# Kernel tuning notes

Measured on AMD Instinct MI355X. Metric: run time of the kernel, lower is better.

## Reference

```python
import jax, jax.numpy as jnp
import numpy as np

B, L, D, H = 8, 512, 512, 8
E, G = 4, 2            # primary experts, ghost experts
THRESH = 0.01          # ghost_activation_threshold
EPS = 1e-5             # LayerNorm eps (torch default)


def _ln(x, s, b):
    m = x.mean(-1, keepdims=True)
    v = ((x - m) ** 2).mean(-1, keepdims=True)
    return (x - m) * jax.lax.rsqrt(v + EPS) * s + b


def _expert(x, ln1_s, ln1_b, wqkv, bqkv, wo, bo, ln2_s, ln2_b, w1, b1, w2, b2):
    # Pre-norm transformer block: MHA + residual, FFN + residual (dropout=0)
    Bn, Ln, Dn = x.shape
    dh = Dn // H
    xn = _ln(x, ln1_s, ln1_b)
    qkv = xn @ wqkv + bqkv                      # [B,L,3D]
    q, k, v = jnp.split(qkv, 3, axis=-1)
    heads = lambda t: t.reshape(Bn, Ln, H, dh).transpose(0, 2, 1, 3)
    q, k, v = heads(q), heads(k), heads(v)      # [B,H,L,dh]
    scores = jnp.einsum('bhqd,bhkd->bhqk', q, k) / np.sqrt(dh).astype(np.float32)
    attn = jax.nn.softmax(scores, axis=-1)
    o = jnp.einsum('bhqk,bhkd->bhqd', attn, v).transpose(0, 2, 1, 3).reshape(Bn, Ln, Dn)
    x = x + o @ wo + bo
    h = _ln(x, ln2_s, ln2_b)
    x = x + jax.nn.gelu(h @ w1 + b1) @ w2 + b2
    return x


def _make_params(key, n, d):
    ks = jax.random.split(key, 4)
    s = 0.02
    return dict(
        ln1_s=jnp.ones((n, d)), ln1_b=jnp.zeros((n, d)),
        wqkv=jax.random.normal(ks[0], (n, d, 3 * d)) * s, bqkv=jnp.zeros((n, 3 * d)),
        wo=jax.random.normal(ks[1], (n, d, d)) * s, bo=jnp.zeros((n, d)),
        ln2_s=jnp.ones((n, d)), ln2_b=jnp.zeros((n, d)),
        w1=jax.random.normal(ks[2], (n, d, 4 * d)) * s, b1=jnp.zeros((n, 4 * d)),
        w2=jax.random.normal(ks[3], (n, 4 * d, d)) * s, b2=jnp.zeros((n, d)))


def setup_inputs() -> dict:
    key = jax.random.key(0)
    k1, k2, k3 = jax.random.split(key, 3)
    inp = {'x': jax.random.normal(k1, (B, L, D), jnp.float32), 'step': 100}
    for pre, n, k in (('p_', E, k2), ('g_', G, k3)):
        for name, arr in _make_params(k, n, D).items():
            inp[pre + name] = arr
    return inp


def reference(x, step,
              p_ln1_s, p_ln1_b, p_wqkv, p_bqkv, p_wo, p_bo, p_ln2_s, p_ln2_b, p_w1, p_b1, p_w2, p_b2,
              g_ln1_s, g_ln1_b, g_wqkv, g_bqkv, g_wo, g_bo, g_ln2_s, g_ln2_b, g_w1, g_b1, g_w2, g_b2):
    pp = (p_ln1_s, p_ln1_b, p_wqkv, p_bqkv, p_wo, p_bo, p_ln2_s, p_ln2_b, p_w1, p_b1, p_w2, p_b2)
    gp = (g_ln1_s, g_ln1_b, g_wqkv, g_bqkv, g_wo, g_bo, g_ln2_s, g_ln2_b, g_w1, g_b1, g_w2, g_b2)
    run = jax.vmap(lambda ps: _expert(x, *ps))
    prim = run(pp)                               # [E,B,L,D]
    # --- saturation metrics (statistics only; detached like .item() in torch) ---
    mean_eo = prim.mean(axis=(1, 2))             # [E,D]
    nrm = mean_eo / jnp.linalg.norm(mean_eo, axis=1, keepdims=True)
    gram = nrm @ nrm.T                           # [E,E]
    ortho = 1.0 - jnp.mean((gram - jnp.eye(E, dtype=gram.dtype)) ** 2)
    recon = prim.mean(axis=0)                    # [B,L,D]
    uvar = jnp.var(x - recon, ddof=1)            # torch.var unbiased default
    sat = jax.lax.stop_gradient(ortho * uvar)
    # --- ghost activation (initial state: all dormant -> ghost 0 gets 0.01) ---
    base = jnp.zeros((G,), x.dtype).at[0].set(0.01)
    rates = jnp.where(sat > THRESH, base, jnp.zeros((G,), x.dtype))
    ghost = jax.vmap(lambda ps: _expert(x, *ps))(gp) * rates[:, None, None, None]  # [G,B,L,D]
    # combine: mean over all (primary + ghost) expert outputs
    out = jnp.concatenate([prim, ghost], axis=0).mean(axis=0)  # [B,L,D]
    return out
```

## Files before the change

### kernel.cpp

```cpp
#include <hip/hip_runtime.h>

typedef __bf16 bf16;
typedef __bf16 bf16x8 __attribute__((ext_vector_type(8)));
typedef float  f32x4  __attribute__((ext_vector_type(4)));

#define AS1 __attribute__((address_space(1)))
#define AS3 __attribute__((address_space(3)))

__device__ __forceinline__ void async16(const void* g, void* l) {
  __builtin_amdgcn_global_load_lds((const AS1 unsigned int*)g, (AS3 unsigned int*)l, 16, 0, 0);
}

__device__ __forceinline__ float gelu_fast(float u) {
  float z = 0.7978845608028654f * (u + 0.044715f * u * u * u);
  z = fminf(fmaxf(z, -15.f), 15.f);
  float t = __expf(2.f * z);
  return u * t / (t + 1.f);
}

template <int FOLD>
__global__ __launch_bounds__(256) void transpose_cvt(
    const float* pbase, const float* gbase, bf16* dst, int K, int M,
    const float* lnsP, const float* lnbP, const float* lnsG, const float* lnbG,
    const float* b0P, const float* b0G, float* bias_eff) {
  __shared__ float tile[32][33];
  const int z = blockIdx.z;
  const float* src = (z < 4) ? pbase + (size_t)z * K * M : gbase;
  bf16* d = dst + (size_t)z * M * K;
  const int mBlk = blockIdx.x * 32, kBlk = blockIdx.y * 32;
  const int tx = threadIdx.x, ty = threadIdx.y;
  for (int i = 0; i < 4; i++)
    tile[ty + i * 8][tx] = src[(size_t)(kBlk + ty + i * 8) * M + mBlk + tx];
  __syncthreads();
  if constexpr (FOLD) {
    const float* s  = (z < 4) ? lnsP + (size_t)z * 512 : lnsG;
    const float* bb = (z < 4) ? lnbP + (size_t)z * 512 : lnbG;
    const float sk = s[kBlk + tx];
    for (int i = 0; i < 4; i++)
      d[(size_t)(mBlk + ty + i * 8) * K + kBlk + tx] = (bf16)(tile[tx][ty + i * 8] * sk);
    if (ty == 0) {
      float acc = 0.f;
      for (int kk = 0; kk < 32; kk++) acc += bb[kBlk + kk] * tile[kk][tx];
      if (kBlk == 0) {
        const float* b0 = (z < 4) ? b0P + (size_t)z * M : b0G;
        acc += b0[mBlk + tx];
      }
      atomicAdd(&bias_eff[(size_t)z * M + mBlk + tx], acc);
    }
  } else {
    for (int i = 0; i < 4; i++)
      d[(size_t)(mBlk + ty + i * 8) * K + kBlk + tx] = (bf16)tile[tx][ty + i * 8];
  }
}

__global__ __launch_bounds__(256) void ln_plain(const float* x, bf16* out) {
  const int t = blockIdx.x, tid = threadIdx.x;
  const float* xr = x + (size_t)t * 512;
  float v0 = xr[tid], v1 = xr[tid + 256];
  float s1 = v0 + v1, s2 = v0 * v0 + v1 * v1;
  for (int off = 32; off > 0; off >>= 1) { s1 += __shfl_down(s1, off); s2 += __shfl_down(s2, off); }
  __shared__ float red[8];
  __shared__ float mv[2];
  if ((tid & 63) == 0) { red[tid >> 6] = s1; red[4 + (tid >> 6)] = s2; }
  __syncthreads();
  if (tid == 0) {
    float a = red[0] + red[1] + red[2] + red[3];
    float b = red[4] + red[5] + red[6] + red[7];
    float mean = a * (1.f / 512.f);
    float var = b * (1.f / 512.f) - mean * mean;
    mv[0] = mean; mv[1] = 1.f / sqrtf(var + 1e-5f);
  }
  __syncthreads();
  const float mean = mv[0], rs = mv[1];
  bf16* o = out + (size_t)t * 512;
  o[tid]       = (bf16)((v0 - mean) * rs);
  o[tid + 256] = (bf16)((v1 - mean) * rs);
}

__global__ __launch_bounds__(256) void ln2_kernel(const bf16* in, const float* sP, const float* bP,
                                                  const float* sG, const float* bG, bf16* out) {
  const int t = blockIdx.x, z = blockIdx.y, tid = threadIdx.x;
  const bf16* xr = in + (size_t)z * 4096 * 512 + (size_t)t * 512;
  float v0 = (float)xr[tid], v1 = (float)xr[tid + 256];
  float s1 = v0 + v1, s2 = v0 * v0 + v1 * v1;
  for (int off = 32; off > 0; off >>= 1) { s1 += __shfl_down(s1, off); s2 += __shfl_down(s2, off); }
  __shared__ float red[8];
  __shared__ float mv[2];
  if ((tid & 63) == 0) { red[tid >> 6] = s1; red[4 + (tid >> 6)] = s2; }
  __syncthreads();
  if (tid == 0) {
    float a = red[0] + red[1] + red[2] + red[3];
    float b = red[4] + red[5] + red[6] + red[7];
    float mean = a * (1.f / 512.f);
    float var = b * (1.f / 512.f) - mean * mean;
    mv[0] = mean; mv[1] = 1.f / sqrtf(var + 1e-5f);
  }
  __syncthreads();
  const float mean = mv[0], rs = mv[1];
  const float* sc = (z < 4) ? sP + (size_t)z * 512 : sG;
  const float* bi = (z < 4) ? bP + (size_t)z * 512 : bG;
  bf16* o = out + (size_t)z * 4096 * 512 + (size_t)t * 512;
  o[tid]       = (bf16)((v0 - mean) * rs * sc[tid] + bi[tid]);
  o[tid + 256] = (bf16)((v1 - mean) * rs * sc[tid + 256] + bi[tid + 256]);
}

template <int MODE>
__global__ __launch_bounds__(256, 2) void gemm_bt(
    const bf16* Abase, long long aStrideZ, const bf16* Wt,
    const float* biasP, const float* biasG, int K, int M,
    bf16* out, const void* resid, long long residStrideZ) {
  const int bx = blockIdx.x, by = blockIdx.y, z = blockIdx.z;
  const bf16* A = Abase + (size_t)z * aStrideZ;
  const bf16* B = Wt + (size_t)z * M * K;
  const float* bias = (z < 4) ? biasP + (size_t)z * M : biasG;
  __shared__ bf16 smem[128 * 136];
  bf16* As = smem;
  bf16* Bs = smem + 128 * 64;
  const int tid = threadIdx.x, wave = tid >> 6, l = tid & 63;
  const int m16 = l & 15, q4 = l >> 4;
  const int wm = wave & 1, wn = wave >> 1;
  f32x4 zero4 = {0.f, 0.f, 0.f, 0.f};
  f32x4 acc[4][4];
  for (int i = 0; i < 4; i++) for (int j = 0; j < 4; j++) acc[i][j] = zero4;
  const int rowA0 = by * 128, rowB0 = bx * 128;

  for (int kt = 0; kt < K; kt += 64) {
    __syncthreads();
    for (int i = 0; i < 4; i++) {
      int s = i * 256 + tid, r = s >> 3, kb = s & 7;
      int col = kt + ((kb ^ (r & 7)) << 3);
      async16(A + (size_t)(rowA0 + r) * K + col, &As[(i * 256 + wave * 64) * 8]);
      async16(B + (size_t)(rowB0 + r) * K + col, &Bs[(i * 256 + wave * 64) * 8]);
    }
    __syncthreads();
    for (int ks = 0; ks < 2; ks++) {
      bf16x8 af[4], bfr[4];
      for (int mi = 0; mi < 4; mi++) {
        int r = wm * 64 + mi * 16 + m16, kb = ks * 4 + q4;
        af[mi] = *(const bf16x8*)&As[r * 64 + ((kb ^ (r & 7)) << 3)];
      }
      for (int ni = 0; ni < 4; ni++) {
        int r = wn * 64 + ni * 16 + m16, kb = ks * 4 + q4;
        bfr[ni] = *(const bf16x8*)&Bs[r * 64 + ((kb ^ (r & 7)) << 3)];
      }
      for (int mi = 0; mi < 4; mi++)
        for (int ni = 0; ni < 4; ni++)
          acc[mi][ni] = __builtin_amdgcn_mfma_f32_16x16x32_bf16(af[mi], bfr[ni], acc[mi][ni], 0, 0, 0);
    }
  }

  __syncthreads();
  for (int ni = 0; ni < 4; ni++) {
    int coll = wn * 64 + ni * 16 + m16;
    float bb = bias[rowB0 + coll];
    for (int mi = 0; mi < 4; mi++) {
      for (int cr = 0; cr < 4; cr++) {
        float v = acc[mi][ni][cr] + bb;
        if constexpr (MODE == 2) v = gelu_fast(v);
        smem[(wm * 64 + mi * 16 + q4 * 4 + cr) * 136 + coll] = (bf16)v;
      }
    }
  }
  __syncthreads();
  bf16* ob = out + (size_t)z * 4096 * M;
  for (int p = 0; p < 8; p++) {
    int r = p * 16 + (tid >> 4), c0 = (tid & 15) * 8;
    bf16x8 vv = *(const bf16x8*)&smem[r * 136 + c0];
    if constexpr (MODE == 1) {
      const float* rx = (const float*)resid + (size_t)(rowA0 + r) * 512 + rowB0 + c0;
      for (int j = 0; j < 8; j++) vv[j] = (bf16)((float)vv[j] + rx[j]);
    } else if constexpr (MODE == 3) {
      const bf16* rx = (const bf16*)resid + (size_t)z * residStrideZ + (size_t)(rowA0 + r) * 512 + rowB0 + c0;
      bf16x8 rv = *(const bf16x8*)rx;
      for (int j = 0; j < 8; j++) vv[j] = (bf16)((float)vv[j] + (float)rv[j]);
    }
    *(bf16x8*)&ob[(size_t)(rowA0 + r) * M + rowB0 + c0] = vv;
  }
}

__global__ __launch_bounds__(256, 2) void attn_kernel(const bf16* qkv, bf16* o) {
  const int qt = blockIdx.x, bh = blockIdx.y, z = blockIdx.z;
  const int b = bh >> 3, h = bh & 7;
  const bf16* base = qkv + (size_t)z * 4096 * 1536 + (size_t)b * 512 * 1536;
  __shared__ bf16 Qs[128 * 64];
  __shared__ bf16 Ks[64 * 64];
  __shared__ bf16 Vt[64 * 72];
  __shared__ bf16 Ps[4][32 * 72];
  const int tid = threadIdx.x, wave = tid >> 6, l = tid & 63;
  const int m16 = l & 15, q4 = l >> 4;
  f32x4 zero4 = {0.f, 0.f, 0.f, 0.f};

  for (int i = 0; i < 4; i++) {
    int s = i * 256 + tid, r = s >> 3, kb = s & 7;
    async16(base + (size_t)(qt * 128 + r) * 1536 + h * 64 + ((kb ^ (r & 7)) << 3),
            &Qs[(i * 256 + wave * 64) * 8]);
  }
  f32x4 Oacc[2][4];
  float m_run[2][4], l_run[2][4];
  for (int rt = 0; rt < 2; rt++)
    for (int cr = 0; cr < 4; cr++) { m_run[rt][cr] = -3.0e38f; l_run[rt][cr] = 0.f; }
  for (int rt = 0; rt < 2; rt++) for (int dt = 0; dt < 4; dt++) Oacc[rt][dt] = zero4;
  __syncthreads();
  bf16x8 qf[2][2];
  for (int rt = 0; rt < 2; rt++)
    for (int ks = 0; ks < 2; ks++) {
      int r = wave * 32 + rt * 16 + m16, kb = ks * 4 + q4;
      qf[rt][ks] = *(const bf16x8*)&Qs[r * 64 + ((kb ^ (r & 7)) << 3)];
    }

  for (int kt = 0; kt < 8; kt++) {
    __syncthreads();
    for (int i = 0; i < 2; i++) {
      int s = i * 256 + tid, r = s >> 3, kb = s & 7;
      async16(base + (size_t)(kt * 64 + r) * 1536 + 512 + h * 64 + ((kb ^ (r & 7)) << 3),
              &Ks[(i * 256 + wave * 64) * 8]);
    }
    for (int p = 0; p < 2; p++) {
      int k = p * 32 + (tid >> 3), d0 = (tid & 7) * 8;
      bf16x8 v8 = *(const bf16x8*)&base[(size_t)(kt * 64 + k) * 1536 + 1024 + h * 64 + d0];
      for (int j = 0; j < 8; j++) Vt[(d0 + j) * 72 + k] = v8[j];
    }
    __syncthreads();
    f32x4 S[2][4];
    for (int rt = 0; rt < 2; rt++)
      for (int ct = 0; ct < 4; ct++) {
        f32x4 a = zero4;
        for (int ks = 0; ks < 2; ks++) {
          int n = ct * 16 + m16, kb = ks * 4 + q4;
          bf16x8 kf = *(const bf16x8*)&Ks[n * 64 + ((kb ^ (n & 7)) << 3)];
          a = __builtin_amdgcn_mfma_f32_16x16x32_bf16(qf[rt][ks], kf, a, 0, 0, 0);
        }
        S[rt][ct] = a * 0.125f;
      }
    float alpha[2][4];
    for (int rt = 0; rt < 2; rt++)
      for (int cr = 0; cr < 4; cr++) {
        float mx = fmaxf(fmaxf(S[rt][0][cr], S[rt][1][cr]), fmaxf(S[rt][2][cr], S[rt][3][cr]));
        mx = fmaxf(mx, __shfl_xor(mx, 1)); mx = fmaxf(mx, __shfl_xor(mx, 2));
        mx = fmaxf(mx, __shfl_xor(mx, 4)); mx = fmaxf(mx, __shfl_xor(mx, 8));
        float mnew = fmaxf(m_run[rt][cr], mx);
        float al = __expf(m_run[rt][cr] - mnew);
        m_run[rt][cr] = mnew;
        float rs = 0.f;
        for (int ct = 0; ct < 4; ct++) {
          float p = __expf(S[rt][ct][cr] - mnew);
          S[rt][ct][cr] = p; rs += p;
        }
        rs += __shfl_xor(rs, 1); rs += __shfl_xor(rs, 2);
        rs += __shfl_xor(rs, 4); rs += __shfl_xor(rs, 8);
        l_run[rt][cr] = l_run[rt][cr] * al + rs;
        alpha[rt][cr] = al;
      }
    for (int rt = 0; rt < 2; rt++)
      for (int dt = 0; dt < 4; dt++)
        for (int cr = 0; cr < 4; cr++) Oacc[rt][dt][cr] *= alpha[rt][cr];
    bf16* pw = &Ps[wave][0];
    for (int rt = 0; rt < 2; rt++)
      for (int ct = 0; ct < 4; ct++)
        for (int cr = 0; cr < 4; cr++)
          pw[(rt * 16 + q4 * 4 + cr) * 72 + ct * 16 + m16] = (bf16)S[rt][ct][cr];
    for (int rt = 0; rt < 2; rt++)
      for (int dt = 0; dt < 4; dt++) {
        f32x4 a = Oacc[rt][dt];
        for (int ks = 0; ks < 2; ks++) {
          bf16x8 pf = *(const bf16x8*)&pw[(rt * 16 + m16) * 72 + ks * 32 + q4 * 8];
          bf16x8 vf = *(const bf16x8*)&Vt[(dt * 16 + m16) * 72 + ks * 32 + q4 * 8];
          a = __builtin_amdgcn_mfma_f32_16x16x32_bf16(pf, vf, a, 0, 0, 0);
        }
        Oacc[rt][dt] = a;
      }
  }
  bf16* ob = o + (size_t)z * 4096 * 512 + (size_t)(b * 512 + qt * 128 + wave * 32) * 512 + h * 64;
  for (int rt = 0; rt < 2; rt++)
    for (int dt = 0; dt < 4; dt++)
      for (int cr = 0; cr < 4; cr++) {
        int r = rt * 16 + q4 * 4 + cr;
        ob[(size_t)r * 512 + dt * 16 + m16] = (bf16)(Oacc[rt][dt][cr] / l_run[rt][cr]);
      }
}

__global__ __launch_bounds__(256) void stats_k(const bf16* eout, const float* x,
                                               float* prim_sum, float* mean_acc, float* accum) {
  const int r0 = blockIdx.x * 32;
  const int tid = threadIdx.x;
  const int c0 = tid * 2;
  float cs[4][2] = {{0.f,0.f},{0.f,0.f},{0.f,0.f},{0.f,0.f}};
  float sd = 0.f, sd2 = 0.f;
  for (int rr = 0; rr < 32; rr++) {
    int row = r0 + rr;
    float s0 = 0.f, s1 = 0.f;
    for (int e = 0; e < 4; e++) {
      const bf16* p = &eout[((size_t)e * 4096 + row) * 512 + c0];
      float f0 = (float)p[0], f1 = (float)p[1];
      cs[e][0] += f0; cs[e][1] += f1;
      s0 += f0; s1 += f1;
    }
    prim_sum[(size_t)row * 512 + c0]     = s0;
    prim_sum[(size_t)row * 512 + c0 + 1] = s1;
    float d0 = x[(size_t)row * 512 + c0]     - s0 * 0.25f;
    float d1 = x[(size_t)row * 512 + c0 + 1] - s1 * 0.25f;
    sd += d0 + d1; sd2 += d0 * d0 + d1 * d1;
  }
  for (int e = 0; e < 4; e++) {
    atomicAdd(&mean_acc[e * 512 + c0],     cs[e][0]);
    atomicAdd(&mean_acc[e * 512 + c0 + 1], cs[e][1]);
  }
  for (int off = 32; off > 0; off >>= 1) { sd += __shfl_down(sd, off); sd2 += __shfl_down(sd2, off); }
  __shared__ float r1[4], r2[4];
  if ((tid & 63) == 0) { r1[tid >> 6] = sd; r2[tid >> 6] = sd2; }
  __syncthreads();
  if (tid == 0) {
    atomicAdd(&accum[0], r1[0] + r1[1] + r1[2] + r1[3]);
    atomicAdd(&accum[1], r2[0] + r2[1] + r2[2] + r2[3]);
  }
}

__global__ void finalize_k(const float* mean_acc, const float* accum, float* rate) {
  const int l = threadIdx.x;
  float me[4][8];
  for (int e = 0; e < 4; e++)
    for (int j = 0; j < 8; j++) me[e][j] = mean_acc[e * 512 + l * 8 + j] * (1.f / 4096.f);
  float dot[4][4];
  for (int e = 0; e < 4; e++)
    for (int f = e; f < 4; f++) {
      float d = 0.f;
      for (int j = 0; j < 8; j++) d += me[e][j] * me[f][j];
      for (int off = 32; off > 0; off >>= 1) d += __shfl_xor(d, off);
      dot[e][f] = d; dot[f][e] = d;
    }
  float nrm[4];
  for (int e = 0; e < 4; e++) nrm[e] = sqrtf(dot[e][e]);
  float acc = 0.f;
  for (int e = 0; e < 4; e++)
    for (int f = 0; f < 4; f++) {
      float g = dot[e][f] / (nrm[e] * nrm[f]) - (e == f ? 1.f : 0.f);
      acc += g * g;
    }
  float ortho = 1.f - acc * (1.f / 16.f);
  float n = 2097152.f;
  float uvar = (accum[1] - accum[0] * accum[0] / n) / (n - 1.f);
  float sat = ortho * uvar;
  if (l == 0) rate[0] = (sat > 0.01f) ? 0.01f : 0.f;
}

__global__ __launch_bounds__(256) void combine_k(const float* prim, const bf16* ghost,
                                                 const float* rate, float* out) {
  float r = rate[0];
  int i = blockIdx.x * 256 + threadIdx.x;
  f32x4 p = ((const f32x4*)prim)[i];
  const bf16* g = ghost + (size_t)i * 4;
  f32x4 o;
  for (int j = 0; j < 4; j++) o[j] = (p[j] + r * (float)g[j]) * (1.f / 6.f);
  ((f32x4*)out)[i] = o;
}

extern "C" void kernel_launch(void* const* d_in, const int* in_sizes, int n_in,
                              void* d_out, int out_size, void* d_ws, size_t ws_size,
                              hipStream_t stream) {
  const float* x       = (const float*)d_in[0];
  const float* p_ln1_s = (const float*)d_in[2];
  const float* p_ln1_b = (const float*)d_in[3];
  const float* p_wqkv  = (const float*)d_in[4];
  const float* p_bqkv  = (const float*)d_in[5];
  const float* p_wo    = (const float*)d_in[6];
  const float* p_bo    = (const float*)d_in[7];
  const float* p_ln2_s = (const float*)d_in[8];
  const float* p_ln2_b = (const float*)d_in[9];
  const float* p_w1    = (const float*)d_in[10];
  const float* p_b1    = (const float*)d_in[11];
  const float* p_w2    = (const float*)d_in[12];
  const float* p_b2    = (const float*)d_in[13];
  const float* g_ln1_s = (const float*)d_in[14];
  const float* g_ln1_b = (const float*)d_in[15];
  const float* g_wqkv  = (const float*)d_in[16];
  const float* g_bqkv  = (const float*)d_in[17];
  const float* g_wo    = (const float*)d_in[18];
  const float* g_bo    = (const float*)d_in[19];
  const float* g_ln2_s = (const float*)d_in[20];
  const float* g_ln2_b = (const float*)d_in[21];
  const float* g_w1    = (const float*)d_in[22];
  const float* g_b1    = (const float*)d_in[23];
  const float* g_w2    = (const float*)d_in[24];
  const float* g_b2    = (const float*)d_in[25];

  char* ws = (char*)d_ws;
  size_t off = 0;
  auto alloc = [&](size_t bytes) { void* p = ws + off; off += (bytes + 255) & ~(size_t)255; return p; };
  bf16* wt_qkv   = (bf16*)alloc(5ull * 1536 * 512 * 2);
  bf16* wt_wo    = (bf16*)alloc(5ull * 512 * 512 * 2);
  bf16* wt_w1    = (bf16*)alloc(5ull * 2048 * 512 * 2);
  bf16* wt_w2    = (bf16*)alloc(5ull * 512 * 2048 * 2);
  bf16* xn       = (bf16*)alloc(4096ull * 512 * 2);
  bf16* act_a    = (bf16*)alloc(5ull * 4096 * 512 * 2);
  bf16* big      = (bf16*)alloc(5ull * 4096 * 2048 * 2);
  bf16* x1       = (bf16*)alloc(5ull * 4096 * 512 * 2);
  bf16* eout     = (bf16*)alloc(5ull * 4096 * 512 * 2);
  float* prim_sum = (float*)alloc(4096ull * 512 * 4);
  float* bias_eff = (float*)alloc(5ull * 1536 * 4);
  float* mean_acc = (float*)alloc(4 * 512 * 4);
  float* accum    = (float*)alloc(256);

  hipMemsetAsync(bias_eff, 0, 5ull * 1536 * 4, stream);
  hipMemsetAsync(mean_acc, 0, 4 * 512 * 4, stream);
  hipMemsetAsync(accum, 0, 16, stream);

  dim3 tb(32, 8);
  transpose_cvt<1><<<dim3(48, 16, 5), tb, 0, stream>>>(p_wqkv, g_wqkv, wt_qkv, 512, 1536,
      p_ln1_s, p_ln1_b, g_ln1_s, g_ln1_b, p_bqkv, g_bqkv, bias_eff);
  transpose_cvt<0><<<dim3(16, 16, 5), tb, 0, stream>>>(p_wo, g_wo, wt_wo, 512, 512,
      nullptr, nullptr, nullptr, nullptr, nullptr, nullptr, nullptr);
  transpose_cvt<0><<<dim3(64, 16, 5), tb, 0, stream>>>(p_w1, g_w1, wt_w1, 512, 2048,
      nullptr, nullptr, nullptr, nullptr, nullptr, nullptr, nullptr);
  transpose_cvt<0><<<dim3(16, 64, 5), tb, 0, stream>>>(p_w2, g_w2, wt_w2, 2048, 512,
      nullptr, nullptr, nullptr, nullptr, nullptr, nullptr, nullptr);

  ln_plain<<<dim3(4096), 256, 0, stream>>>(x, xn);
  gemm_bt<0><<<dim3(12, 32, 5), 256, 0, stream>>>(xn, 0, wt_qkv, bias_eff, bias_eff + 4ull * 1536,
                                                  512, 1536, big, nullptr, 0);
  attn_kernel<<<dim3(4, 64, 5), 256, 0, stream>>>(big, act_a);
  gemm_bt<1><<<dim3(4, 32, 5), 256, 0, stream>>>(act_a, 4096ll * 512, wt_wo, p_bo, g_bo,
                                                 512, 512, x1, x, 0);
  ln2_kernel<<<dim3(4096, 5), 256, 0, stream>>>(x1, p_ln2_s, p_ln2_b, g_ln2_s, g_ln2_b, act_a);
  gemm_bt<2><<<dim3(16, 32, 5), 256, 0, stream>>>(act_a, 4096ll * 512, wt_w1, p_b1, g_b1,
                                                  512, 2048, big, nullptr, 0);
  gemm_bt<3><<<dim3(4, 32, 5), 256, 0, stream>>>(big, 4096ll * 2048, wt_w2, p_b2, g_b2,
                                                 2048, 512, eout, x1, 4096ll * 512);
  stats_k<<<dim3(128), 256, 0, stream>>>(eout, x, prim_sum, mean_acc, accum);
  finalize_k<<<1, 64, 0, stream>>>(mean_acc, accum, accum + 2);
  combine_k<<<dim3(2048), 256, 0, stream>>>(prim_sum, eout + 4ull * 4096 * 512, accum + 2, (float*)d_out);
}
```

Measured before the change: 509.5 us.

## Use 32x32x16 MFMA in GEMM and stage V asynchronously through LDS

The GEMM inner loop switches from 16x16x32 MFMA tiles to 32x32x16 MFMA tiles, with four 16-wide accumulators per wave. This cuts the number of LDS fragment loads per MFMA and the instruction count, and the epilogue row mapping is rewritten to match the new output layout. In attention, V is now loaded with async global-to-LDS copies and transposed inside LDS instead of being read from global memory and scattered into LDS. The shared buffers are merged so that the Q staging area is reused for K and V. This adds one extra barrier per key tile.

```diff
diff --git a/kernel.cpp b/kernel.cpp
--- a/kernel.cpp
+++ b/kernel.cpp
@@ -3,6 +3,7 @@
 typedef __bf16 bf16;
 typedef __bf16 bf16x8 __attribute__((ext_vector_type(8)));
 typedef float  f32x4  __attribute__((ext_vector_type(4)));
+typedef float  f32x16 __attribute__((ext_vector_type(16)));
 
 #define AS1 __attribute__((address_space(1)))
 #define AS3 __attribute__((address_space(3)))
@@ -117,11 +118,11 @@
   bf16* As = smem;
   bf16* Bs = smem + 128 * 64;
   const int tid = threadIdx.x, wave = tid >> 6, l = tid & 63;
-  const int m16 = l & 15, q4 = l >> 4;
+  const int l31 = l & 31, lh = l >> 5;
   const int wm = wave & 1, wn = wave >> 1;
-  f32x4 zero4 = {0.f, 0.f, 0.f, 0.f};
-  f32x4 acc[4][4];
-  for (int i = 0; i < 4; i++) for (int j = 0; j < 4; j++) acc[i][j] = zero4;
+  f32x16 acc[2][2];
+  for (int i = 0; i < 2; i++) for (int j = 0; j < 2; j++)
+    for (int r = 0; r < 16; r++) acc[i][j][r] = 0.f;
   const int rowA0 = by * 128, rowB0 = bx * 128;
 
   for (int kt = 0; kt < K; kt += 64) {
@@ -133,34 +134,34 @@
       async16(B + (size_t)(rowB0 + r) * K + col, &Bs[(i * 256 + wave * 64) * 8]);
     }
     __syncthreads();
-    for (int ks = 0; ks < 2; ks++) {
-      bf16x8 af[4], bfr[4];
-      for (int mi = 0; mi < 4; mi++) {
-        int r = wm * 64 + mi * 16 + m16, kb = ks * 4 + q4;
-        af[mi] = *(const bf16x8*)&As[r * 64 + ((kb ^ (r & 7)) << 3)];
-      }
-      for (int ni = 0; ni < 4; ni++) {
-        int r = wn * 64 + ni * 16 + m16, kb = ks * 4 + q4;
-        bfr[ni] = *(const bf16x8*)&Bs[r * 64 + ((kb ^ (r & 7)) << 3)];
-      }
-      for (int mi = 0; mi < 4; mi++)
-        for (int ni = 0; ni < 4; ni++)
-          acc[mi][ni] = __builtin_amdgcn_mfma_f32_16x16x32_bf16(af[mi], bfr[ni], acc[mi][ni], 0, 0, 0);
-    }
-  }
-
-  __syncthreads();
-  for (int ni = 0; ni < 4; ni++) {
-    int coll = wn * 64 + ni * 16 + m16;
-    float bb = bias[rowB0 + coll];
-    for (int mi = 0; mi < 4; mi++) {
-      for (int cr = 0; cr < 4; cr++) {
-        float v = acc[mi][ni][cr] + bb;
+    for (int ks = 0; ks < 4; ks++) {
+      bf16x8 af[2], bfr[2];
+      for (int ti = 0; ti < 2; ti++) {
+        int r = wm * 64 + ti * 32 + l31, kb = (ks * 2 + lh) ^ (r & 7);
+        af[ti] = *(const bf16x8*)&As[r * 64 + (kb << 3)];
+      }
+      for (int ni = 0; ni < 2; ni++) {
+        int r = wn * 64 + ni * 32 + l31, kb = (ks * 2 + lh) ^ (r & 7);
+        bfr[ni] = *(const bf16x8*)&Bs[r * 64 + (kb << 3)];
+      }
+      for (int ti = 0; ti < 2; ti++)
+        for (int ni = 0; ni < 2; ni++)
+          acc[ti][ni] = __builtin_amdgcn_mfma_f32_32x32x16_bf16(af[ti], bfr[ni], acc[ti][ni], 0, 0, 0);
+    }
+  }
+
+  __syncthreads();
+  for (int ti = 0; ti < 2; ti++)
+    for (int ni = 0; ni < 2; ni++) {
+      int coll = wn * 64 + ni * 32 + l31;
+      float bb = bias[rowB0 + coll];
+      for (int reg = 0; reg < 16; reg++) {
+        int row = wm * 64 + ti * 32 + (reg & 3) + 8 * (reg >> 2) + 4 * lh;
+        float v = acc[ti][ni][reg] + bb;
         if constexpr (MODE == 2) v = gelu_fast(v);
-        smem[(wm * 64 + mi * 16 + q4 * 4 + cr) * 136 + coll] = (bf16)v;
-      }
-    }
-  }
+        smem[row * 136 + coll] = (bf16)v;
+      }
+    }
   __syncthreads();
   bf16* ob = out + (size_t)z * 4096 * M;
   for (int p = 0; p < 8; p++) {
@@ -182,18 +183,19 @@
   const int qt = blockIdx.x, bh = blockIdx.y, z = blockIdx.z;
   const int b = bh >> 3, h = bh & 7;
   const bf16* base = qkv + (size_t)z * 4096 * 1536 + (size_t)b * 512 * 1536;
-  __shared__ bf16 Qs[128 * 64];
-  __shared__ bf16 Ks[64 * 64];
-  __shared__ bf16 Vt[64 * 72];
-  __shared__ bf16 Ps[4][32 * 72];
+  __shared__ bf16 smem[22016];
+  bf16* Ks = smem;
+  bf16* Vs = smem + 4096;
+  bf16* Vt = smem + 8192;
   const int tid = threadIdx.x, wave = tid >> 6, l = tid & 63;
   const int m16 = l & 15, q4 = l >> 4;
+  bf16* pw = smem + 12800 + wave * 32 * 72;
   f32x4 zero4 = {0.f, 0.f, 0.f, 0.f};
 
   for (int i = 0; i < 4; i++) {
     int s = i * 256 + tid, r = s >> 3, kb = s & 7;
     async16(base + (size_t)(qt * 128 + r) * 1536 + h * 64 + ((kb ^ (r & 7)) << 3),
-            &Qs[(i * 256 + wave * 64) * 8]);
+            &smem[(i * 256 + wave * 64) * 8]);
   }
   f32x4 Oacc[2][4];
   float m_run[2][4], l_run[2][4];
@@ -205,7 +207,7 @@
   for (int rt = 0; rt < 2; rt++)
     for (int ks = 0; ks < 2; ks++) {
       int r = wave * 32 + rt * 16 + m16, kb = ks * 4 + q4;
-      qf[rt][ks] = *(const bf16x8*)&Qs[r * 64 + ((kb ^ (r & 7)) << 3)];
+      qf[rt][ks] = *(const bf16x8*)&smem[r * 64 + ((kb ^ (r & 7)) << 3)];
     }
 
   for (int kt = 0; kt < 8; kt++) {
@@ -214,11 +216,18 @@
       int s = i * 256 + tid, r = s >> 3, kb = s & 7;
       async16(base + (size_t)(kt * 64 + r) * 1536 + 512 + h * 64 + ((kb ^ (r & 7)) << 3),
               &Ks[(i * 256 + wave * 64) * 8]);
-    }
-    for (int p = 0; p < 2; p++) {
-      int k = p * 32 + (tid >> 3), d0 = (tid & 7) * 8;
-      bf16x8 v8 = *(const bf16x8*)&base[(size_t)(kt * 64 + k) * 1536 + 1024 + h * 64 + d0];
-      for (int j = 0; j < 8; j++) Vt[(d0 + j) * 72 + k] = v8[j];
+      async16(base + (size_t)(kt * 64 + r) * 1536 + 1024 + h * 64 + (kb << 3),
+              &Vs[(i * 256 + wave * 64) * 8]);
+    }
+    __syncthreads();
+    {
+      int d = tid & 63, kb2 = (tid >> 6) * 16;
+      for (int g = 0; g < 2; g++) {
+        int kbase = kb2 + g * 8;
+        bf16 tmp[8];
+        for (int j = 0; j < 8; j++) tmp[j] = Vs[(kbase + j) * 64 + d];
+        *(bf16x8*)&Vt[d * 72 + kbase] = *(const bf16x8*)tmp;
+      }
     }
     __syncthreads();
     f32x4 S[2][4];
@@ -226,8 +235,8 @@
       for (int ct = 0; ct < 4; ct++) {
         f32x4 a = zero4;
         for (int ks = 0; ks < 2; ks++) {
-          int n = ct * 16 + m16, kb = ks * 4 + q4;
-          bf16x8 kf = *(const bf16x8*)&Ks[n * 64 + ((kb ^ (n & 7)) << 3)];
+          int n = ct * 16 + m16, kb = (ks * 4 + q4) ^ (n & 7);
+          bf16x8 kf = *(const bf16x8*)&Ks[n * 64 + (kb << 3)];
           a = __builtin_amdgcn_mfma_f32_16x16x32_bf16(qf[rt][ks], kf, a, 0, 0, 0);
         }
         S[rt][ct] = a * 0.125f;
@@ -254,7 +263,6 @@
     for (int rt = 0; rt < 2; rt++)
       for (int dt = 0; dt < 4; dt++)
         for (int cr = 0; cr < 4; cr++) Oacc[rt][dt][cr] *= alpha[rt][cr];
-    bf16* pw = &Ps[wave][0];
     for (int rt = 0; rt < 2; rt++)
       for (int ct = 0; ct < 4; ct++)
         for (int cr = 0; cr < 4; cr++)
```

After: 490.9 us. -3.7%, faster.
